# Kernel tuning notes

Hardware: AMD Instinct MI355X
Metric: run time of the kernel (lower is better)

Reference implementation:

```python
import jax, jax.numpy as jnp
import numpy as np

BATCH, QLEN, KVLEN = 4, 8, 512
C, H = 512, 8
N = C // H  # 64
D_W, D_A, D_V, D_G = 32, 32, 32, 96
GN_EPS = 1e-5 * 8 ** 2  # head_size_divisor = 8


def setup_inputs() -> dict:
    key = jax.random.key(0)
    ks = jax.random.split(key, 32)
    rn = lambda i, sh, s=1.0: jax.random.normal(ks[i], sh, dtype=jnp.float32) * s
    ru = lambda i, sh: jax.random.uniform(ks[i], sh, dtype=jnp.float32)
    s = C ** -0.5
    return {
        "query": rn(0, (BATCH, QLEN, C)),
        "keyval": rn(1, (BATCH, KVLEN, C)),
        "v_first": rn(2, (BATCH * QLEN, KVLEN, C)),
        "x_r": ru(3, (1, 1, C)), "x_w": ru(4, (1, 1, C)), "x_k": ru(5, (1, 1, C)),
        "x_v": ru(6, (1, 1, C)), "x_a": ru(7, (1, 1, C)), "x_g": ru(8, (1, 1, C)),
        "w0": jnp.linspace(-7.0, -2.0, C, dtype=jnp.float32).reshape(1, 1, C) + 0.5,
        "w1": rn(9, (C, D_W), 0.02), "w2": rn(10, (D_W, C), 0.02),
        "a0": rn(11, (1, 1, C), 0.01), "a1": rn(12, (C, D_A), 0.02), "a2": rn(13, (D_A, C), 0.02),
        "v0": jnp.ones((1, 1, C), jnp.float32), "v1": rn(14, (C, D_V), 0.02), "v2": rn(15, (D_V, C), 0.02),
        "g1": rn(16, (C, D_G), 0.02), "g2": rn(17, (D_G, C), 0.02),
        "k_k": 0.85 + rn(18, (1, 1, C), 0.02), "k_a": jnp.ones((1, 1, C), jnp.float32),
        "r_k": rn(19, (H, N), 0.02),
        "Wr": rn(20, (C, C), 0.5 * s), "Wk": rn(21, (C, C), 0.05 * s),
        "Wv": rn(22, (C, C), 0.5 * s), "Wo": rn(23, (C, C), s),
        "ln_w": 1.0 + rn(24, (C,), 0.02), "ln_b": rn(25, (C,), 0.02),
    }


def _rwkv7_scan(r, w, k, v, a, b):
    # r,w,k,v,a,b: [B,T,C]; RWKV7 generalized delta rule, state [B,H,N,N] (value x key).
    B, T, _ = r.shape
    toTBHN = lambda t: t.reshape(B, T, H, N).transpose(1, 0, 2, 3)  # [T,B,H,N]
    rT, kT, vT, aT, bT = map(toTBHN, (r, k, v, a, b))
    wT = jnp.exp(-jnp.exp(toTBHN(w)))  # decay in (0,1)

    def step(state, xs):
        r_t, w_t, k_t, v_t, a_t, b_t = xs
        sa = jnp.einsum('bhij,bhj->bhi', state, a_t)  # state @ a
        state = (state * w_t[:, :, None, :]
                 + sa[..., None] * b_t[:, :, None, :]
                 + v_t[..., None] * k_t[:, :, None, :])
        out = jnp.einsum('bhij,bhj->bhi', state, r_t)
        return state, out

    state0 = jnp.zeros((B, H, N, N), dtype=jnp.float32)
    _, outs = jax.lax.scan(step, state0, (rT, wT, kT, vT, aT, bT))
    return outs.transpose(1, 0, 2, 3).reshape(B, T, C)  # [B,T,C]


def _forward(query, keyval, v_first, x_r, x_w, x_k, x_v, x_a, x_g,
             w0, w1, w2, a0, a1, a2, v0, v1, v2, g1, g2,
             k_k, k_a, r_k, Wr, Wk, Wv, Wo, ln_w, ln_b):
    batch, qlen, Cc = query.shape
    kvlen = keyval.shape[1]
    # cross-product expansion: every (query token, keyval sequence) pair
    eq = jnp.repeat(query[:, :, None, :], kvlen, axis=2).reshape(-1, kvlen, Cc)
    ek = jnp.repeat(keyval[:, None, :, :], qlen, axis=1).reshape(-1, kvlen, Cc)
    B, T = ek.shape[0], kvlen
    xx_cross = eq - ek
    shifted = jnp.pad(ek, ((0, 0), (1, 0), (0, 0)))[:, :-1]  # time_shift
    xx_kv = shifted - ek
    x = ek
    xr = x + xx_cross * x_r
    xw = x + xx_cross * x_w
    xa = x + xx_cross * x_a
    xg = x + xx_cross * x_g
    xk = x + xx_kv * x_k
    xv = x + xx_kv * x_v

    r = xr @ Wr
    w = -jax.nn.softplus(-(w0 + jnp.tanh(xw @ w1) @ w2)) - 0.5
    k = xk @ Wk
    v = xv @ Wv
    v = v + (v_first - v) * jax.nn.sigmoid(v0 + (xv @ v1) @ v2)  # layer_id != 0
    a = jax.nn.sigmoid(a0 + (xa @ a1) @ a2)
    g = jax.nn.sigmoid(xg @ g1) @ g2

    kk = k * k_k
    kkh = kk.reshape(B, T, H, N)
    kkh = kkh / jnp.maximum(jnp.linalg.norm(kkh, axis=-1, keepdims=True), 1e-12)
    kk = kkh.reshape(B, T, Cc)
    k = k * (1.0 + (a - 1.0) * k_a)

    xo = _rwkv7_scan(r, w, k, v, -kk, kk * a)

    # GroupNorm over H groups of N channels, eps = 1e-5 * head_size_divisor^2
    y = xo.reshape(B * T, H, N)
    mu = y.mean(axis=-1, keepdims=True)
    var = y.var(axis=-1, keepdims=True)
    yn = (y - mu) * jax.lax.rsqrt(var + GN_EPS)
    xo = (yn.reshape(B * T, Cc) * ln_w + ln_b).reshape(B, T, Cc)

    rk = (r.reshape(B, T, H, N) * k.reshape(B, T, H, N) * r_k).sum(axis=-1, keepdims=True)
    xo = xo + (rk * v.reshape(B, T, H, N)).reshape(B, T, Cc)
    xo = xo * g
    xo = xo[:, -1, :]  # frames=None path
    xo = xo.reshape(batch, qlen, Cc) @ Wo
    return xo, v_first


def reference(query, keyval, v_first, x_r, x_w, x_k, x_v, x_a, x_g,
              w0, w1, w2, a0, a1, a2, v0, v1, v2, g1, g2,
              k_k, k_a, r_k, Wr, Wk, Wv, Wo, ln_w, ln_b):
    return _forward(query, keyval, v_first, x_r, x_w, x_k, x_v, x_a, x_g,
                    w0, w1, w2, a0, a1, a2, v0, v1, v2, g1, g2,
                    k_k, k_a, r_k, Wr, Wk, Wv, Wo, ln_w, ln_b)
```

## Files before the change

kernel.cpp:

```cpp
#include <hip/hip_runtime.h>
#include <cstdint>

#define TT 512
#define CC 512
#define HH 8
#define NN 64
#define BQ 32
#define NB 4
#define TG 128

__device__ __forceinline__ float sigm(float x){ return 1.f/(1.f+__expf(-x)); }

__device__ __forceinline__ float wsum(float x){
  #pragma unroll
  for (int o=32;o;o>>=1) x += __shfl_xor(x, o, 64);
  return x;
}

template<int NR>
__device__ __forceinline__ void rowsum64_batch(float* x){
  #pragma unroll
  for (int i=0;i<NR;i++)
    x[i] += __int_as_float(__builtin_amdgcn_mov_dpp(__float_as_int(x[i]), 0x121, 0xf, 0xf, true));
  #pragma unroll
  for (int i=0;i<NR;i++)
    x[i] += __int_as_float(__builtin_amdgcn_mov_dpp(__float_as_int(x[i]), 0x122, 0xf, 0xf, true));
  #pragma unroll
  for (int i=0;i<NR;i++)
    x[i] += __int_as_float(__builtin_amdgcn_mov_dpp(__float_as_int(x[i]), 0x124, 0xf, 0xf, true));
  #pragma unroll
  for (int i=0;i<NR;i++)
    x[i] += __int_as_float(__builtin_amdgcn_mov_dpp(__float_as_int(x[i]), 0x128, 0xf, 0xf, true));
  float y[NR];
  #pragma unroll
  for (int i=0;i<NR;i++) asm("v_mov_b32 %0, %1" : "=v"(y[i]) : "v"(x[i]));
  #pragma unroll
  for (int i=0;i<NR;i++) asm("v_permlane16_swap_b32 %0, %1" : "+v"(x[i]), "+v"(y[i]));
  #pragma unroll
  for (int i=0;i<NR;i++) x[i] += y[i];
  #pragma unroll
  for (int i=0;i<NR;i++) asm("v_mov_b32 %0, %1" : "=v"(y[i]) : "v"(x[i]));
  #pragma unroll
  for (int i=0;i<NR;i++) asm("v_permlane32_swap_b32 %0, %1" : "+v"(x[i]), "+v"(y[i]));
  #pragma unroll
  for (int i=0;i<NR;i++) x[i] += y[i];
}

__global__ __launch_bounds__(256) void k_prep(
  const float* __restrict__ q, const float* __restrict__ kv,
  const float* __restrict__ x_r, const float* __restrict__ x_w,
  const float* __restrict__ x_a, const float* __restrict__ x_g,
  const float* __restrict__ w1, const float* __restrict__ a1,
  const float* __restrict__ g1,
  float* __restrict__ Qw, float* __restrict__ Qa,
  float* __restrict__ ghw, float* __restrict__ xrw)
{
  int bq = blockIdx.x, b = bq >> 3, tid = threadIdx.x;
  int wave = tid >> 6, lane = tid & 63;
  __shared__ float qxw[CC], qxa[CC], sxg[CC];
  for (int c = tid; c < CC; c += 256){
    float qv = q[bq*CC + c];
    float kl = kv[((size_t)b*TT + (TT-1))*CC + c];
    xrw[bq*CC + c] = kl + (qv - kl)*x_r[c];
    sxg[c] = kl + (qv - kl)*x_g[c];
    qxw[c] = qv*x_w[c];
    qxa[c] = qv*x_a[c];
  }
  __syncthreads();
  for (int dot = wave; dot < 160; dot += 4){
    const float* buf; const float* W; int ld, dd;
    if (dot < 32)      { buf = qxw; W = w1; ld = 32; dd = dot; }
    else if (dot < 64) { buf = qxa; W = a1; ld = 32; dd = dot-32; }
    else               { buf = sxg; W = g1; ld = 96; dd = dot-64; }
    float s = 0.f;
    #pragma unroll
    for (int m = 0; m < 8; m++){
      int c = m*64 + lane;
      s = fmaf(buf[c], W[c*ld + dd], s);
    }
    s = wsum(s);
    if (lane == 0){
      if (dot < 32)      Qw[bq*32 + dd] = s;
      else if (dot < 64) Qa[bq*32 + dd] = s;
      else               ghw[bq*96 + dd] = sigm(s);
    }
  }
}

__global__ __launch_bounds__(256) void k_rg(
  const float* __restrict__ xrw, const float* __restrict__ ghw,
  const float* __restrict__ Wr, const float* __restrict__ g2,
  float* __restrict__ rrow, float* __restrict__ grow)
{
  int bq = blockIdx.y; int co0 = blockIdx.x*64;
  int tid = threadIdx.x, tx = tid & 63, ty = tid >> 6;
  __shared__ float sxr[CC];
  __shared__ float sgh[96];
  __shared__ float red[4][64];
  sxr[tid]     = xrw[bq*CC + tid];
  sxr[tid+256] = xrw[bq*CC + tid + 256];
  if (tid < 96) sgh[tid] = ghw[bq*96 + tid];
  __syncthreads();
  float p = 0.f;
  for (int i = 0; i < 128; i++){
    int c = ty*128 + i;
    p = fmaf(sxr[c], Wr[(size_t)c*CC + co0 + tx], p);
  }
  red[ty][tx] = p;
  float pg = 0.f;
  for (int d = ty*24; d < ty*24 + 24; d++)
    pg = fmaf(sgh[d], g2[(size_t)d*CC + co0 + tx], pg);
  __syncthreads();
  if (ty == 0)
    rrow[bq*CC + co0 + tx] = (red[0][tx]+red[1][tx])+(red[2][tx]+red[3][tx]);
  __syncthreads();
  red[ty][tx] = pg;
  __syncthreads();
  if (ty == 0)
    grow[bq*CC + co0 + tx] = (red[0][tx]+red[1][tx])+(red[2][tx]+red[3][tx]);
}

__global__ __launch_bounds__(256) void k_shift(
  const float* __restrict__ kv, const float* __restrict__ x_k,
  const float* __restrict__ x_v,
  float* __restrict__ xk, float* __restrict__ xv)
{
  int g = blockIdx.x*256 + threadIdx.x;
  int bt = g >> 7, t = bt & (TT-1), c4 = g & 127;
  const float4* kv4 = (const float4*)kv;
  float4 cur = kv4[g];
  float4 sh  = t ? kv4[g-128] : make_float4(0.f,0.f,0.f,0.f);
  float4 kc  = ((const float4*)x_k)[c4];
  float4 vc  = ((const float4*)x_v)[c4];
  float4 ok, ov;
  ok.x = cur.x + (sh.x-cur.x)*kc.x; ov.x = cur.x + (sh.x-cur.x)*vc.x;
  ok.y = cur.y + (sh.y-cur.y)*kc.y; ov.y = cur.y + (sh.y-cur.y)*vc.y;
  ok.z = cur.z + (sh.z-cur.z)*kc.z; ov.z = cur.z + (sh.z-cur.z)*vc.z;
  ok.w = cur.w + (sh.w-cur.w)*kc.w; ov.w = cur.w + (sh.w-cur.w)*vc.w;
  ((float4*)xk)[g] = ok;
  ((float4*)xv)[g] = ov;
}

__global__ __launch_bounds__(256) void k_pgemm(
  const float* __restrict__ kv, const float* __restrict__ xv,
  const float* __restrict__ x_w, const float* __restrict__ x_a,
  const float* __restrict__ w1, const float* __restrict__ a1,
  const float* __restrict__ v1,
  float* __restrict__ Pw, float* __restrict__ Pa, float* __restrict__ HV)
{
  int mat = blockIdx.y;
  int r0 = blockIdx.x * 64;
  const float* A = (mat == 2) ? xv : kv;
  const float* B = (mat == 0) ? w1 : (mat == 1) ? a1 : v1;
  float* O       = (mat == 0) ? Pw : (mat == 1) ? Pa : HV;
  int tid = threadIdx.x;
  __shared__ float As[32][65];
  __shared__ float Bs[32][32];
  __shared__ float scl[CC];
  for (int c = tid; c < CC; c += 256)
    scl[c] = (mat == 0) ? (1.f - x_w[c]) : (mat == 1) ? (1.f - x_a[c]) : 1.f;
  __syncthreads();
  int tx = tid & 31, ty = tid >> 5;
  float acc[8];
  #pragma unroll
  for (int i = 0; i < 8; i++) acc[i] = 0.f;
  for (int k0 = 0; k0 < 512; k0 += 32){
    #pragma unroll
    for (int p = 0; p < 8; p++){
      int e = tid + p*256;
      int kk2 = e & 31, r = e >> 5;
      As[kk2][r] = A[(size_t)(r0+r)*512 + k0 + kk2] * scl[k0 + kk2];
    }
    #pragma unroll
    for (int p = 0; p < 4; p++){
      int e = tid + p*256;
      int n = e & 31, kk2 = e >> 5;
      Bs[kk2][n] = B[(size_t)(k0+kk2)*32 + n];
    }
    __syncthreads();
    #pragma unroll
    for (int kk2 = 0; kk2 < 32; kk2++){
      float bb = Bs[kk2][tx];
      #pragma unroll
      for (int i = 0; i < 8; i++)
        acc[i] = fmaf(As[kk2][ty*8 + i], bb, acc[i]);
    }
    __syncthreads();
  }
  #pragma unroll
  for (int i = 0; i < 8; i++)
    O[(size_t)(r0 + ty*8 + i)*32 + tx] = acc[i];
}

__global__ __launch_bounds__(256) void k_svpack(
  const float* __restrict__ HV, const float* __restrict__ v2,
  const float* __restrict__ v0, const float* __restrict__ kkg,
  float* __restrict__ svP, float* __restrict__ kkP)
{
  int blk = blockIdx.x;
  int b = blk >> 7, tg = blk & (TG-1);
  int tid = threadIdx.x;
  __shared__ float hv[4][32];
  if (tid < 128){
    int u = tid >> 5, d = tid & 31;
    hv[u][d] = HV[((size_t)(b*TT + tg*4 + u))*32 + d];
  }
  __syncthreads();
  #pragma unroll
  for (int cc = 0; cc < 2; cc++){
    int c = tid + cc*256;
    int h = c >> 6, cc0 = c & 63;
    float vcol[32];
    #pragma unroll
    for (int d = 0; d < 32; d++) vcol[d] = v2[d*CC + c];
    float v0c = v0[c];
    float sres[4], kres[4];
    #pragma unroll
    for (int u = 0; u < 4; u++){
      float s = 0.f;
      #pragma unroll
      for (int d = 0; d < 32; d++) s = fmaf(hv[u][d], vcol[d], s);
      sres[u] = sigm(v0c + s);
      kres[u] = kkg[((size_t)(b*TT + tg*4 + u))*CC + c];
    }
    size_t o = ((size_t)(b*HH + h)*TG + tg)*64 + cc0;
    ((float4*)svP)[o] = make_float4(sres[0],sres[1],sres[2],sres[3]);
    ((float4*)kkP)[o] = make_float4(kres[0],kres[1],kres[2],kres[3]);
  }
}

__global__ __launch_bounds__(256) void gemm2(
  const float* __restrict__ A0, const float* __restrict__ W0, float* __restrict__ C0,
  const float* __restrict__ A1, const float* __restrict__ W1, float* __restrict__ vpP)
{
  __shared__ float As[32][68];
  __shared__ float Bs[32][64];
  int z = blockIdx.z;
  const float* A = z ? A1 : A0;
  const float* W = z ? W1 : W0;
  int tid = threadIdx.x;
  int tx = tid & 15, ty = tid >> 4;
  int m0 = blockIdx.y*64, n0 = blockIdx.x*64;
  float acc[4][4];
  #pragma unroll
  for (int i=0;i<4;i++)
    #pragma unroll
    for (int j=0;j<4;j++) acc[i][j]=0.f;

  for (int k0 = 0; k0 < 512; k0 += 32){
    #pragma unroll
    for (int i = 0; i < 8; i++){
      int e = tid + i*256;
      int kk = e & 31, m = e >> 5;
      As[kk][m] = A[(size_t)(m0+m)*512 + k0 + kk];
    }
    #pragma unroll
    for (int i = 0; i < 8; i++){
      int e = tid + i*256;
      int n = e & 63, kk = e >> 6;
      Bs[kk][n] = W[(size_t)(k0+kk)*512 + n0 + n];
    }
    __syncthreads();
    #pragma unroll
    for (int kk = 0; kk < 32; kk++){
      float a4[4], b4[4];
      #pragma unroll
      for (int i=0;i<4;i++) a4[i] = As[kk][ty*4+i];
      #pragma unroll
      for (int j=0;j<4;j++) b4[j] = Bs[kk][tx*4+j];
      #pragma unroll
      for (int i=0;i<4;i++)
        #pragma unroll
        for (int j=0;j<4;j++) acc[i][j] += a4[i]*b4[j];
    }
    __syncthreads();
  }
  if (z == 0){
    #pragma unroll
    for (int i=0;i<4;i++)
      #pragma unroll
      for (int j=0;j<4;j++)
        C0[(size_t)(m0+ty*4+i)*512 + n0 + tx*4 + j] = acc[i][j];
  } else {
    int m = m0 + ty*4;
    int b = m >> 9, t = m & (TT-1), tg = t >> 2;
    int h = n0 >> 6;
    float4* dst = (float4*)vpP + ((size_t)(b*HH + h)*TG + tg)*64 + tx*4;
    #pragma unroll
    for (int j=0;j<4;j++)
      dst[j] = make_float4(acc[0][j],acc[1][j],acc[2][j],acc[3][j]);
  }
}

__global__ __launch_bounds__(512) void k_kk(
  const float* __restrict__ kg, const float* __restrict__ k_k,
  float* __restrict__ kkg)
{
  int bt = blockIdx.x, tid = threadIdx.x;
  float v = kg[(size_t)bt*CC + tid]*k_k[tid];
  float ss = wsum(v*v);
  float nrm = fmaxf(sqrtf(ss), 1e-12f);
  kkg[(size_t)bt*CC + tid] = v/nrm;
}

__global__ __launch_bounds__(512) void k_wkb(
  const float* __restrict__ Pw, const float* __restrict__ Pa,
  const float* __restrict__ Qw, const float* __restrict__ Qa,
  const float* __restrict__ w2, const float* __restrict__ a2,
  const float* __restrict__ w0, const float* __restrict__ a0,
  const float* __restrict__ k_a, const float* __restrict__ kg,
  const float* __restrict__ kkg,
  float* __restrict__ wP, float* __restrict__ kP, float* __restrict__ bP)
{
  int blk = blockIdx.x;
  int bq = blk >> 7, tg = blk & (TG-1), t0 = tg*4, b = bq >> 3;
  int tid = threadIdx.x;
  __shared__ float sth[4][32], sal[4][32];
  if (tid < 256){
    int g = (tid >> 5) & 3, d = tid & 31;
    int pidx = ((b << 9) | (t0 + g))*32 + d;
    if (tid < 128) sth[g][d] = tanhf(Pw[pidx] + Qw[bq*32 + d]);
    else           sal[g][d] = Pa[pidx] + Qa[bq*32 + d];
  }
  __syncthreads();
  int c = tid, h = c >> 6, cc0 = c & 63;
  float wreg[32], areg[32];
  #pragma unroll
  for (int d = 0; d < 32; d++){ wreg[d] = w2[d*CC + c]; areg[d] = a2[d*CC + c]; }
  float w0c = w0[c], a0c = a0[c], kac = k_a[c];
  float w4a[4], k4a[4], b4a[4];
  #pragma unroll
  for (int g = 0; g < 4; g++){
    float wa = 0.f, aa = 0.f;
    #pragma unroll
    for (int d = 0; d < 32; d++){
      wa = fmaf(sth[g][d], wreg[d], wa);
      aa = fmaf(sal[g][d], areg[d], aa);
    }
    float a_sig = sigm(a0c + aa);
    float wdec  = __expf(-0.60653066f * sigm(w0c + wa));
    size_t bt = (size_t)((b << 9) | (t0 + g));
    float kvv = kg[bt*CC + c];
    float kkv = kkg[bt*CC + c];
    w4a[g] = wdec;
    k4a[g] = kvv*(1.f + (a_sig - 1.f)*kac);
    b4a[g] = kkv*a_sig;
  }
  size_t o = ((size_t)(bq*HH + h)*TG + tg)*64 + cc0;
  ((float4*)wP)[o] = make_float4(w4a[0],w4a[1],w4a[2],w4a[3]);
  ((float4*)kP)[o] = make_float4(k4a[0],k4a[1],k4a[2],k4a[3]);
  ((float4*)bP)[o] = make_float4(b4a[0],b4a[1],b4a[2],b4a[3]);
}

#define SCAN_STEP(wc,kc,bc,ac,pc,sc,vfc) do{ \
  float vj = fmaf((vfc)-(pc), (sc), (pc)); \
  float rr[2]; rr[0]=(kc)*g; rr[1]=(bc)*g; \
  rowsum64_batch<2>(rr); \
  out = fmaf(rr[0], vj, out); \
  g = fmaf((wc), g, -((ac)*rr[1])); }while(0)

__global__ __launch_bounds__(64, 1) void k_scan(
  const float* __restrict__ wP, const float* __restrict__ kP,
  const float* __restrict__ bP, const float* __restrict__ kkP,
  const float* __restrict__ vpP, const float* __restrict__ svP,
  const float* __restrict__ vfirst,
  const float* __restrict__ rrow, const float* __restrict__ grow,
  const float* __restrict__ r_k, const float* __restrict__ ln_w,
  const float* __restrict__ ln_b, float* __restrict__ xo)
{
  int blk = blockIdx.x; int bq = blk >> 3, h = blk & 7, b = bq >> 3;
  int lane = threadIdx.x & 63;

  const float4* wp4 = (const float4*)wP  + ((size_t)(bq*HH + h))*TG*64 + lane;
  const float4* kp4 = (const float4*)kP  + ((size_t)(bq*HH + h))*TG*64 + lane;
  const float4* bp4 = (const float4*)bP  + ((size_t)(bq*HH + h))*TG*64 + lane;
  const float4* ap4 = (const float4*)kkP + ((size_t)(b*HH + h))*TG*64 + lane;
  const float4* pp4 = (const float4*)vpP + ((size_t)(b*HH + h))*TG*64 + lane;
  const float4* sp4 = (const float4*)svP + ((size_t)(b*HH + h))*TG*64 + lane;
  const float*  pvf = vfirst + (size_t)bq*TT*CC + h*NN + lane;

  float g   = rrow[(size_t)bq*CC + h*NN + lane];
  float out = 0.f;

  constexpr int PD = 4;
  float4 fw[PD], fk[PD], fb[PD], fa[PD], fp[PD], fs[PD];
  float fv0[PD], fv1[PD], fv2[PD], fv3[PD];
  #pragma unroll
  for (int d = 0; d < PD; ++d){
    int gg = TG-1 - d; int go = gg*64;
    fw[d]=wp4[go]; fk[d]=kp4[go]; fb[d]=bp4[go]; fa[d]=ap4[go];
    fp[d]=pp4[go]; fs[d]=sp4[go];
    const float* pv = pvf + (size_t)(4*gg)*CC;
    fv0[d]=pv[0]; fv1[d]=pv[CC]; fv2[d]=pv[2*CC]; fv3[d]=pv[3*CC];
  }

  #pragma unroll 1
  for (int gb = 0; gb < TG; gb += PD){
    #pragma unroll
    for (int sl = 0; sl < PD; ++sl){
      int gi = TG-1 - (gb + sl);
      float4 w4=fw[sl], k4=fk[sl], b4=fb[sl], a4=fa[sl], p4=fp[sl], s4=fs[sl];
      float v3=fv3[sl], v2_=fv2[sl], v1_=fv1[sl], v0_=fv0[sl];
      int gp = gi - PD; gp = gp < 0 ? 0 : gp; int go = gp*64;
      fw[sl]=wp4[go]; fk[sl]=kp4[go]; fb[sl]=bp4[go]; fa[sl]=ap4[go];
      fp[sl]=pp4[go]; fs[sl]=sp4[go];
      { const float* pv = pvf + (size_t)(4*gp)*CC;
        fv0[sl]=pv[0]; fv1[sl]=pv[CC]; fv2[sl]=pv[2*CC]; fv3[sl]=pv[3*CC]; }
      __builtin_amdgcn_sched_barrier(0);
      SCAN_STEP(w4.w,k4.w,b4.w,a4.w,p4.w,s4.w,v3);
      SCAN_STEP(w4.z,k4.z,b4.z,a4.z,p4.z,s4.z,v2_);
      SCAN_STEP(w4.y,k4.y,b4.y,a4.y,p4.y,s4.y,v1_);
      SCAN_STEP(w4.x,k4.x,b4.x,a4.x,p4.x,s4.x,v0_);
    }
  }

  {
    float mean = wsum(out) * (1.f/NN);
    float dv = out - mean;
    float var = wsum(dv*dv) * (1.f/NN);
    float yn = dv * rsqrtf(var + 6.4e-4f);
    int c = h*NN + lane;
    float y2 = yn * ln_w[c] + ln_b[c];
    int goT = (TG-1)*64;
    float kl  = kp4[goT].w;
    float rl  = rrow[(size_t)bq*CC + c];
    float rk  = wsum(rl*kl*r_k[c]);
    float vp_ = pp4[goT].w, sv_ = sp4[goT].w;
    float vf_ = pvf[(size_t)(TT-1)*CC];
    float v_i = vp_ + (vf_ - vp_)*sv_;
    float res = (y2 + rk*v_i) * grow[(size_t)bq*CC + c];
    xo[bq*CC + c] = res;
  }
}

__global__ __launch_bounds__(256) void k_out(
  const float* __restrict__ xo, const float* __restrict__ Wo,
  float* __restrict__ outp)
{
  int bq = blockIdx.y; int co0 = blockIdx.x*64;
  int tid = threadIdx.x, tx = tid & 63, ty = tid >> 6;
  __shared__ float row[CC];
  __shared__ float red[4][64];
  row[tid]     = xo[bq*CC + tid];
  row[tid+256] = xo[bq*CC + tid + 256];
  __syncthreads();
  float p = 0.f;
  for (int i = 0; i < 128; i++){
    int c = ty*128 + i;
    p = fmaf(row[c], Wo[(size_t)c*CC + co0 + tx], p);
  }
  red[ty][tx] = p;
  __syncthreads();
  if (ty == 0)
    outp[bq*CC + co0 + tx] = (red[0][tx]+red[1][tx])+(red[2][tx]+red[3][tx]);
}

extern "C" void kernel_launch(void* const* d_in, const int* in_sizes, int n_in,
                              void* d_out, int out_size, void* d_ws, size_t ws_size,
                              hipStream_t stream)
{
  const float* q   = (const float*)d_in[0];
  const float* kv  = (const float*)d_in[1];
  const float* vf  = (const float*)d_in[2];
  const float* x_r = (const float*)d_in[3];
  const float* x_w = (const float*)d_in[4];
  const float* x_k = (const float*)d_in[5];
  const float* x_v = (const float*)d_in[6];
  const float* x_a = (const float*)d_in[7];
  const float* x_g = (const float*)d_in[8];
  const float* w0  = (const float*)d_in[9];
  const float* w1  = (const float*)d_in[10];
  const float* w2  = (const float*)d_in[11];
  const float* a0  = (const float*)d_in[12];
  const float* a1  = (const float*)d_in[13];
  const float* a2  = (const float*)d_in[14];
  const float* v0  = (const float*)d_in[15];
  const float* v1  = (const float*)d_in[16];
  const float* v2  = (const float*)d_in[17];
  const float* g1  = (const float*)d_in[18];
  const float* g2  = (const float*)d_in[19];
  const float* k_k = (const float*)d_in[20];
  const float* k_a = (const float*)d_in[21];
  const float* r_k = (const float*)d_in[22];
  const float* Wr  = (const float*)d_in[23];
  const float* Wk  = (const float*)d_in[24];
  const float* Wv  = (const float*)d_in[25];
  const float* Wo  = (const float*)d_in[26];
  const float* lnw = (const float*)d_in[27];
  const float* lnb = (const float*)d_in[28];
  float* outp = (float*)d_out;
  float* ws = (float*)d_ws;

  float* xk  = ws + 0;
  float* xv  = ws + 1048576;
  float* kg  = ws + 2097152;
  float* vpP = ws + 3145728;
  float* svP = ws + 4194304;
  float* kkg = ws + 5242880;
  float* Pw  = ws + 6291456;
  float* Pa  = ws + 6356992;
  float* Qw  = ws + 6422528;
  float* Qa  = ws + 6423552;
  float* HV  = ws + 6424576;
  float* rr  = ws + 7473152;
  float* gr  = ws + 7489536;
  float* xo  = ws + 7505920;
  float* wP  = ws + 7522304;
  float* kP  = ws + 15910912;
  float* bP  = ws + 24299520;
  float* xrw = ws + 32688128;
  float* ghw = ws + 32704512;
  float* kkP = xk;

  hipMemcpyAsync(outp + BQ*CC, vf,
                 (size_t)BQ*TT*CC*sizeof(float), hipMemcpyDeviceToDevice, stream);

  k_prep<<<32, 256, 0, stream>>>(q, kv, x_r, x_w, x_a, x_g, w1, a1, g1,
                                 Qw, Qa, ghw, xrw);
  k_rg<<<dim3(8, 32), 256, 0, stream>>>(xrw, ghw, Wr, g2, rr, gr);
  k_shift<<<1024, 256, 0, stream>>>(kv, x_k, x_v, xk, xv);
  gemm2<<<dim3(8, 32, 2), 256, 0, stream>>>(xk, Wk, kg, xv, Wv, vpP);
  k_pgemm<<<dim3(32, 3), 256, 0, stream>>>(kv, xv, x_w, x_a, w1, a1, v1,
                                           Pw, Pa, HV);
  k_kk<<<NB*TT, 512, 0, stream>>>(kg, k_k, kkg);
  k_svpack<<<NB*TG, 256, 0, stream>>>(HV, v2, v0, kkg, svP, kkP);
  k_wkb<<<BQ*TG, 512, 0, stream>>>(Pw, Pa, Qw, Qa, w2, a2, w0, a0, k_a,
                                   kg, kkg, wP, kP, bP);
  k_scan<<<BQ*HH, 64, 0, stream>>>(wP, kP, bP, kkP, vpP, svP, vf, rr, gr, r_k,
                                   lnw, lnb, xo);
  k_out<<<dim3(8, 32), 256, 0, stream>>>(xo, Wo, outp);
}
```

Measured before the change: 360.2 us.

## Pair scan steps algebraically and fuse kk-normalization into packed sv kernel

The backward scan now advances two timesteps per iteration. It batches six cross-lane DPP reductions at once instead of two reductions per step, which shortens the serial dependency chain. The k and b terms are no longer precomputed per query batch; the scan rebuilds them from per-batch kg/kk plus a, cutting the per-bq packed arrays from three to two. gemm2 now writes kg in packed layout, and a new k_svn kernel fuses the kk L2 normalization with the v-gate sigmoid, removing the k_kk and k_svpack launches. The cost is extra per-step arithmetic in the scan and a reordering of floating-point operations.

```diff
diff --git a/kernel.cpp b/kernel.cpp
--- a/kernel.cpp
+++ b/kernel.cpp
@@ -192,45 +192,8 @@
     O[(size_t)(r0 + ty*8 + i)*32 + tx] = acc[i];
 }
 
-__global__ __launch_bounds__(256) void k_svpack(
-  const float* __restrict__ HV, const float* __restrict__ v2,
-  const float* __restrict__ v0, const float* __restrict__ kkg,
-  float* __restrict__ svP, float* __restrict__ kkP)
-{
-  int blk = blockIdx.x;
-  int b = blk >> 7, tg = blk & (TG-1);
-  int tid = threadIdx.x;
-  __shared__ float hv[4][32];
-  if (tid < 128){
-    int u = tid >> 5, d = tid & 31;
-    hv[u][d] = HV[((size_t)(b*TT + tg*4 + u))*32 + d];
-  }
-  __syncthreads();
-  #pragma unroll
-  for (int cc = 0; cc < 2; cc++){
-    int c = tid + cc*256;
-    int h = c >> 6, cc0 = c & 63;
-    float vcol[32];
-    #pragma unroll
-    for (int d = 0; d < 32; d++) vcol[d] = v2[d*CC + c];
-    float v0c = v0[c];
-    float sres[4], kres[4];
-    #pragma unroll
-    for (int u = 0; u < 4; u++){
-      float s = 0.f;
-      #pragma unroll
-      for (int d = 0; d < 32; d++) s = fmaf(hv[u][d], vcol[d], s);
-      sres[u] = sigm(v0c + s);
-      kres[u] = kkg[((size_t)(b*TT + tg*4 + u))*CC + c];
-    }
-    size_t o = ((size_t)(b*HH + h)*TG + tg)*64 + cc0;
-    ((float4*)svP)[o] = make_float4(sres[0],sres[1],sres[2],sres[3]);
-    ((float4*)kkP)[o] = make_float4(kres[0],kres[1],kres[2],kres[3]);
-  }
-}
-
 __global__ __launch_bounds__(256) void gemm2(
-  const float* __restrict__ A0, const float* __restrict__ W0, float* __restrict__ C0,
+  const float* __restrict__ A0, const float* __restrict__ W0, float* __restrict__ kgP,
   const float* __restrict__ A1, const float* __restrict__ W1, float* __restrict__ vpP)
 {
   __shared__ float As[32][68];
@@ -275,42 +238,63 @@
     }
     __syncthreads();
   }
-  if (z == 0){
-    #pragma unroll
-    for (int i=0;i<4;i++)
-      #pragma unroll
-      for (int j=0;j<4;j++)
-        C0[(size_t)(m0+ty*4+i)*512 + n0 + tx*4 + j] = acc[i][j];
-  } else {
-    int m = m0 + ty*4;
-    int b = m >> 9, t = m & (TT-1), tg = t >> 2;
-    int h = n0 >> 6;
-    float4* dst = (float4*)vpP + ((size_t)(b*HH + h)*TG + tg)*64 + tx*4;
-    #pragma unroll
-    for (int j=0;j<4;j++)
-      dst[j] = make_float4(acc[0][j],acc[1][j],acc[2][j],acc[3][j]);
-  }
-}
-
-__global__ __launch_bounds__(512) void k_kk(
-  const float* __restrict__ kg, const float* __restrict__ k_k,
-  float* __restrict__ kkg)
-{
-  int bt = blockIdx.x, tid = threadIdx.x;
-  float v = kg[(size_t)bt*CC + tid]*k_k[tid];
-  float ss = wsum(v*v);
-  float nrm = fmaxf(sqrtf(ss), 1e-12f);
-  kkg[(size_t)bt*CC + tid] = v/nrm;
-}
-
-__global__ __launch_bounds__(512) void k_wkb(
+  int m = m0 + ty*4;
+  int b = m >> 9, t = m & (TT-1), tg = t >> 2;
+  int h = n0 >> 6;
+  float* dstB = z ? vpP : kgP;
+  float4* dst = (float4*)dstB + ((size_t)(b*HH + h)*TG + tg)*64 + tx*4;
+  #pragma unroll
+  for (int j=0;j<4;j++)
+    dst[j] = make_float4(acc[0][j],acc[1][j],acc[2][j],acc[3][j]);
+}
+
+__global__ __launch_bounds__(512) void k_svn(
+  const float* __restrict__ HV, const float* __restrict__ v2,
+  const float* __restrict__ v0, const float* __restrict__ k_k,
+  const float* __restrict__ kgP,
+  float* __restrict__ svP, float* __restrict__ kkP)
+{
+  int blk = blockIdx.x;
+  int b = blk >> 7, tg = blk & (TG-1);
+  int tid = threadIdx.x;
+  __shared__ float hv[4][32];
+  if (tid < 128){
+    int u = tid >> 5, d = tid & 31;
+    hv[u][d] = HV[((size_t)(b*TT + tg*4 + u))*32 + d];
+  }
+  __syncthreads();
+  int c = tid, h = c >> 6, cc0 = c & 63;
+  size_t o = ((size_t)(b*HH + h)*TG + tg)*64 + cc0;
+  float4 kg4 = ((const float4*)kgP)[o];
+  float kkc = k_k[c];
+  float q0 = kg4.x*kkc, q1 = kg4.y*kkc, q2 = kg4.z*kkc, q3 = kg4.w*kkc;
+  float ss[4] = {q0*q0, q1*q1, q2*q2, q3*q3};
+  rowsum64_batch<4>(ss);
+  float4 kkq;
+  kkq.x = q0 / fmaxf(sqrtf(ss[0]), 1e-12f);
+  kkq.y = q1 / fmaxf(sqrtf(ss[1]), 1e-12f);
+  kkq.z = q2 / fmaxf(sqrtf(ss[2]), 1e-12f);
+  kkq.w = q3 / fmaxf(sqrtf(ss[3]), 1e-12f);
+  ((float4*)kkP)[o] = kkq;
+  float v0c = v0[c];
+  float s0 = v0c, s1 = v0c, s2 = v0c, s3 = v0c;
+  #pragma unroll
+  for (int d = 0; d < 32; d++){
+    float vc = v2[d*CC + c];
+    s0 = fmaf(hv[0][d], vc, s0);
+    s1 = fmaf(hv[1][d], vc, s1);
+    s2 = fmaf(hv[2][d], vc, s2);
+    s3 = fmaf(hv[3][d], vc, s3);
+  }
+  ((float4*)svP)[o] = make_float4(sigm(s0), sigm(s1), sigm(s2), sigm(s3));
+}
+
+__global__ __launch_bounds__(512) void k_wa(
   const float* __restrict__ Pw, const float* __restrict__ Pa,
   const float* __restrict__ Qw, const float* __restrict__ Qa,
   const float* __restrict__ w2, const float* __restrict__ a2,
   const float* __restrict__ w0, const float* __restrict__ a0,
-  const float* __restrict__ k_a, const float* __restrict__ kg,
-  const float* __restrict__ kkg,
-  float* __restrict__ wP, float* __restrict__ kP, float* __restrict__ bP)
+  float* __restrict__ wP, float* __restrict__ aP)
 {
   int blk = blockIdx.x;
   int bq = blk >> 7, tg = blk & (TG-1), t0 = tg*4, b = bq >> 3;
@@ -327,8 +311,8 @@
   float wreg[32], areg[32];
   #pragma unroll
   for (int d = 0; d < 32; d++){ wreg[d] = w2[d*CC + c]; areg[d] = a2[d*CC + c]; }
-  float w0c = w0[c], a0c = a0[c], kac = k_a[c];
-  float w4a[4], k4a[4], b4a[4];
+  float w0c = w0[c], a0c = a0[c];
+  float w4a[4], a4a[4];
   #pragma unroll
   for (int g = 0; g < 4; g++){
     float wa = 0.f, aa = 0.f;
@@ -337,58 +321,59 @@
       wa = fmaf(sth[g][d], wreg[d], wa);
       aa = fmaf(sal[g][d], areg[d], aa);
     }
-    float a_sig = sigm(a0c + aa);
-    float wdec  = __expf(-0.60653066f * sigm(w0c + wa));
-    size_t bt = (size_t)((b << 9) | (t0 + g));
-    float kvv = kg[bt*CC + c];
-    float kkv = kkg[bt*CC + c];
-    w4a[g] = wdec;
-    k4a[g] = kvv*(1.f + (a_sig - 1.f)*kac);
-    b4a[g] = kkv*a_sig;
+    w4a[g] = __expf(-0.60653066f * sigm(w0c + wa));
+    a4a[g] = sigm(a0c + aa);
   }
   size_t o = ((size_t)(bq*HH + h)*TG + tg)*64 + cc0;
   ((float4*)wP)[o] = make_float4(w4a[0],w4a[1],w4a[2],w4a[3]);
-  ((float4*)kP)[o] = make_float4(k4a[0],k4a[1],k4a[2],k4a[3]);
-  ((float4*)bP)[o] = make_float4(b4a[0],b4a[1],b4a[2],b4a[3]);
-}
-
-#define SCAN_STEP(wc,kc,bc,ac,pc,sc,vfc) do{ \
-  float vj = fmaf((vfc)-(pc), (sc), (pc)); \
-  float rr[2]; rr[0]=(kc)*g; rr[1]=(bc)*g; \
-  rowsum64_batch<2>(rr); \
-  out = fmaf(rr[0], vj, out); \
-  g = fmaf((wc), g, -((ac)*rr[1])); }while(0)
+  ((float4*)aP)[o] = make_float4(a4a[0],a4a[1],a4a[2],a4a[3]);
+}
+
+#define SCAN_PAIR(wh,ah,gh,nh,vh, wl,al,gl,nl,vl) do{ \
+  float kh = (gh)*fmaf((ah)-1.f, kac, 1.f), bh = (nh)*(ah); \
+  float klo = (gl)*fmaf((al)-1.f, kac, 1.f), blo = (nl)*(al); \
+  float u = (wh)*g; \
+  float dd[6]; \
+  dd[0]=kh*g; dd[1]=bh*g; dd[2]=klo*u; dd[3]=blo*u; dd[4]=klo*(nh); dd[5]=blo*(nh); \
+  rowsum64_batch<6>(dd); \
+  out = fmaf(dd[0], (vh), out); \
+  g   = fmaf(-dd[1], (nh), u); \
+  out = fmaf(fmaf(-dd[4], dd[1], dd[2]), (vl), out); \
+  g   = fmaf(-fmaf(-dd[5], dd[1], dd[3]), (nl), (wl)*g); \
+}while(0)
 
 __global__ __launch_bounds__(64, 1) void k_scan(
-  const float* __restrict__ wP, const float* __restrict__ kP,
-  const float* __restrict__ bP, const float* __restrict__ kkP,
+  const float* __restrict__ wP, const float* __restrict__ aP,
+  const float* __restrict__ kgP, const float* __restrict__ kkP,
   const float* __restrict__ vpP, const float* __restrict__ svP,
   const float* __restrict__ vfirst,
   const float* __restrict__ rrow, const float* __restrict__ grow,
-  const float* __restrict__ r_k, const float* __restrict__ ln_w,
-  const float* __restrict__ ln_b, float* __restrict__ xo)
+  const float* __restrict__ r_k, const float* __restrict__ k_a,
+  const float* __restrict__ ln_w, const float* __restrict__ ln_b,
+  float* __restrict__ xo)
 {
   int blk = blockIdx.x; int bq = blk >> 3, h = blk & 7, b = bq >> 3;
   int lane = threadIdx.x & 63;
 
   const float4* wp4 = (const float4*)wP  + ((size_t)(bq*HH + h))*TG*64 + lane;
-  const float4* kp4 = (const float4*)kP  + ((size_t)(bq*HH + h))*TG*64 + lane;
-  const float4* bp4 = (const float4*)bP  + ((size_t)(bq*HH + h))*TG*64 + lane;
-  const float4* ap4 = (const float4*)kkP + ((size_t)(b*HH + h))*TG*64 + lane;
+  const float4* ap4 = (const float4*)aP  + ((size_t)(bq*HH + h))*TG*64 + lane;
+  const float4* gp4 = (const float4*)kgP + ((size_t)(b*HH + h))*TG*64 + lane;
+  const float4* np4 = (const float4*)kkP + ((size_t)(b*HH + h))*TG*64 + lane;
   const float4* pp4 = (const float4*)vpP + ((size_t)(b*HH + h))*TG*64 + lane;
   const float4* sp4 = (const float4*)svP + ((size_t)(b*HH + h))*TG*64 + lane;
   const float*  pvf = vfirst + (size_t)bq*TT*CC + h*NN + lane;
 
+  float kac = k_a[h*NN + lane];
   float g   = rrow[(size_t)bq*CC + h*NN + lane];
   float out = 0.f;
 
   constexpr int PD = 4;
-  float4 fw[PD], fk[PD], fb[PD], fa[PD], fp[PD], fs[PD];
+  float4 fw[PD], fa[PD], fg[PD], fn[PD], fp[PD], fs[PD];
   float fv0[PD], fv1[PD], fv2[PD], fv3[PD];
   #pragma unroll
   for (int d = 0; d < PD; ++d){
     int gg = TG-1 - d; int go = gg*64;
-    fw[d]=wp4[go]; fk[d]=kp4[go]; fb[d]=bp4[go]; fa[d]=ap4[go];
+    fw[d]=wp4[go]; fa[d]=ap4[go]; fg[d]=gp4[go]; fn[d]=np4[go];
     fp[d]=pp4[go]; fs[d]=sp4[go];
     const float* pv = pvf + (size_t)(4*gg)*CC;
     fv0[d]=pv[0]; fv1[d]=pv[CC]; fv2[d]=pv[2*CC]; fv3[d]=pv[3*CC];
@@ -399,18 +384,20 @@
     #pragma unroll
     for (int sl = 0; sl < PD; ++sl){
       int gi = TG-1 - (gb + sl);
-      float4 w4=fw[sl], k4=fk[sl], b4=fb[sl], a4=fa[sl], p4=fp[sl], s4=fs[sl];
-      float v3=fv3[sl], v2_=fv2[sl], v1_=fv1[sl], v0_=fv0[sl];
+      float4 w4=fw[sl], a4=fa[sl], g4=fg[sl], n4=fn[sl], p4=fp[sl], s4=fs[sl];
+      float x3=fv3[sl], x2=fv2[sl], x1=fv1[sl], x0=fv0[sl];
       int gp = gi - PD; gp = gp < 0 ? 0 : gp; int go = gp*64;
-      fw[sl]=wp4[go]; fk[sl]=kp4[go]; fb[sl]=bp4[go]; fa[sl]=ap4[go];
+      fw[sl]=wp4[go]; fa[sl]=ap4[go]; fg[sl]=gp4[go]; fn[sl]=np4[go];
       fp[sl]=pp4[go]; fs[sl]=sp4[go];
       { const float* pv = pvf + (size_t)(4*gp)*CC;
         fv0[sl]=pv[0]; fv1[sl]=pv[CC]; fv2[sl]=pv[2*CC]; fv3[sl]=pv[3*CC]; }
       __builtin_amdgcn_sched_barrier(0);
-      SCAN_STEP(w4.w,k4.w,b4.w,a4.w,p4.w,s4.w,v3);
-      SCAN_STEP(w4.z,k4.z,b4.z,a4.z,p4.z,s4.z,v2_);
-      SCAN_STEP(w4.y,k4.y,b4.y,a4.y,p4.y,s4.y,v1_);
-      SCAN_STEP(w4.x,k4.x,b4.x,a4.x,p4.x,s4.x,v0_);
+      float v3 = fmaf(x3 - p4.w, s4.w, p4.w);
+      float v2_ = fmaf(x2 - p4.z, s4.z, p4.z);
+      float v1_ = fmaf(x1 - p4.y, s4.y, p4.y);
+      float v0_ = fmaf(x0 - p4.x, s4.x, p4.x);
+      SCAN_PAIR(w4.w,a4.w,g4.w,n4.w,v3,  w4.z,a4.z,g4.z,n4.z,v2_);
+      SCAN_PAIR(w4.y,a4.y,g4.y,n4.y,v1_, w4.x,a4.x,g4.x,n4.x,v0_);
     }
   }
 
@@ -422,12 +409,13 @@
     int c = h*NN + lane;
     float y2 = yn * ln_w[c] + ln_b[c];
     int goT = (TG-1)*64;
-    float kl  = kp4[goT].w;
+    float4 kgT = gp4[goT]; float4 aT = ap4[goT];
+    float kl  = kgT.w * fmaf(aT.w - 1.f, kac, 1.f);
     float rl  = rrow[(size_t)bq*CC + c];
     float rk  = wsum(rl*kl*r_k[c]);
     float vp_ = pp4[goT].w, sv_ = sp4[goT].w;
     float vf_ = pvf[(size_t)(TT-1)*CC];
-    float v_i = vp_ + (vf_ - vp_)*sv_;
+    float v_i = fmaf(vf_ - vp_, sv_, vp_);
     float res = (y2 + rk*v_i) * grow[(size_t)bq*CC + c];
     xo[bq*CC + c] = res;
   }
@@ -493,10 +481,10 @@
 
   float* xk  = ws + 0;
   float* xv  = ws + 1048576;
-  float* kg  = ws + 2097152;
+  float* kgP = ws + 2097152;
   float* vpP = ws + 3145728;
   float* svP = ws + 4194304;
-  float* kkg = ws + 5242880;
+  float* kkP = ws + 5242880;
   float* Pw  = ws + 6291456;
   float* Pa  = ws + 6356992;
   float* Qw  = ws + 6422528;
@@ -506,11 +494,9 @@
   float* gr  = ws + 7489536;
   float* xo  = ws + 7505920;
   float* wP  = ws + 7522304;
-  float* kP  = ws + 15910912;
-  float* bP  = ws + 24299520;
+  float* aP  = ws + 15910912;
   float* xrw = ws + 32688128;
   float* ghw = ws + 32704512;
-  float* kkP = xk;
 
   hipMemcpyAsync(outp + BQ*CC, vf,
                  (size_t)BQ*TT*CC*sizeof(float), hipMemcpyDeviceToDevice, stream);
@@ -519,14 +505,12 @@
                                  Qw, Qa, ghw, xrw);
   k_rg<<<dim3(8, 32), 256, 0, stream>>>(xrw, ghw, Wr, g2, rr, gr);
   k_shift<<<1024, 256, 0, stream>>>(kv, x_k, x_v, xk, xv);
-  gemm2<<<dim3(8, 32, 2), 256, 0, stream>>>(xk, Wk, kg, xv, Wv, vpP);
+  gemm2<<<dim3(8, 32, 2), 256, 0, stream>>>(xk, Wk, kgP, xv, Wv, vpP);
   k_pgemm<<<dim3(32, 3), 256, 0, stream>>>(kv, xv, x_w, x_a, w1, a1, v1,
                                            Pw, Pa, HV);
-  k_kk<<<NB*TT, 512, 0, stream>>>(kg, k_k, kkg);
-  k_svpack<<<NB*TG, 256, 0, stream>>>(HV, v2, v0, kkg, svP, kkP);
-  k_wkb<<<BQ*TG, 512, 0, stream>>>(Pw, Pa, Qw, Qa, w2, a2, w0, a0, k_a,
-                                   kg, kkg, wP, kP, bP);
-  k_scan<<<BQ*HH, 64, 0, stream>>>(wP, kP, bP, kkP, vpP, svP, vf, rr, gr, r_k,
-                                   lnw, lnb, xo);
+  k_svn<<<NB*TG, 512, 0, stream>>>(HV, v2, v0, k_k, kgP, svP, kkP);
+  k_wa<<<BQ*TG, 512, 0, stream>>>(Pw, Pa, Qw, Qa, w2, a2, w0, a0, wP, aP);
+  k_scan<<<BQ*HH, 64, 0, stream>>>(wP, aP, kgP, kkP, vpP, svP, vf, rr, gr,
+                                   r_k, k_a, lnw, lnb, xo);
   k_out<<<dim3(8, 32), 256, 0, stream>>>(xo, Wo, outp);
 }
```

After: 369.2 us. +2.5%, slower.
